# Kernel optimization log

Measured on AMD Instinct MI355X. Metric: run time of the kernel, lower is better.

## Reference

```python
import jax, jax.numpy as jnp
import numpy as np

EPS = 1e-8  # torch.cosine_similarity norm clamp

def setup_inputs() -> dict:
    key = jax.random.key(0)
    k1, k2, k3, k4 = jax.random.split(key, 4)
    B, S, D, C = 64, 512, 768, 512
    V = jax.random.normal(k1, (B, S, D), dtype=jnp.float32)
    label_embeddings = jax.random.normal(k2, (C, D), dtype=jnp.float32)
    fc_w = jax.random.normal(k3, (C, D), dtype=jnp.float32) * 0.02
    fc_b = jax.random.normal(k4, (C,), dtype=jnp.float32) * 0.02
    return {"V": V, "label_embeddings": label_embeddings, "fc_w": fc_w, "fc_b": fc_b}

def reference(V, label_embeddings, fc_w, fc_b):
    # Normalized embeddings (cosine similarity = dot of unit vectors, norms clamped at EPS)
    Vn = V / jnp.maximum(jnp.linalg.norm(V, axis=-1, keepdims=True), EPS)
    Ln = label_embeddings / jnp.maximum(
        jnp.linalg.norm(label_embeddings, axis=-1, keepdims=True), EPS)
    # [B, S, C] cosine similarities, then max over classes -> per-token weight m [B, S]
    sims = jnp.einsum('bsd,cd->bsc', Vn, Ln)
    m = jnp.max(sims, axis=-1)
    # Softmax over sequence dim -> attention beta [B, S]
    beta = jax.nn.softmax(m, axis=-1)
    # Weighted sum of token embeddings: z = V^T beta  -> [B, D]
    z = jnp.einsum('bsd,bs->bd', V, beta)
    # Final classifier
    out = z @ fc_w.T + fc_b
    return (out, z)
```

## Files before the change

### kernel.cpp

```cpp
#include <hip/hip_runtime.h>
#include <cstdint>
#include <cstddef>

#define BB 64
#define SS 512
#define DD 768
#define CC 512

typedef __attribute__((ext_vector_type(8))) short short8;
typedef __attribute__((ext_vector_type(4))) float f32x4;

#define GLOBAL_AS __attribute__((address_space(1)))
#define LDS_AS __attribute__((address_space(3)))

static __device__ __forceinline__ unsigned short f2bf(float f) {
  union { float f; unsigned u; } v; v.f = f;
  unsigned u = v.u;
  u += 0x7FFFu + ((u >> 16) & 1u);
  return (unsigned short)(u >> 16);
}
static __device__ __forceinline__ float bf2f(unsigned short u) {
  union { unsigned u; float f; } v; v.u = ((unsigned)u) << 16; return v.f;
}

static __device__ __forceinline__ void async_copy16(const void* g, void* l) {
  __builtin_amdgcn_global_load_lds((const GLOBAL_AS void*)g, (LDS_AS void*)l,
                                   16, 0, 0);
}

__global__ __launch_bounds__(256) void k_label_norm(const float* __restrict__ L,
                                                    unsigned short* __restrict__ Lnb) {
  const int c = blockIdx.x;
  const int tid = threadIdx.x;
  const float* row = L + (size_t)c * DD;
  float v[3];
  float s = 0.f;
#pragma unroll
  for (int k = 0; k < 3; k++) { v[k] = row[tid + 256 * k]; s += v[k] * v[k]; }
#pragma unroll
  for (int o = 32; o > 0; o >>= 1) s += __shfl_xor(s, o, 64);
  __shared__ float wsum[4];
  if ((tid & 63) == 0) wsum[tid >> 6] = s;
  __syncthreads();
  const float tot = wsum[0] + wsum[1] + wsum[2] + wsum[3];
  const float inv = 1.f / fmaxf(sqrtf(tot), 1e-8f);
  unsigned short* orow = Lnb + (size_t)c * DD;
  const int sw = c & 7;
#pragma unroll
  for (int k = 0; k < 3; k++) {
    const int d = tid + 256 * k;
    const int idx = (((d >> 3) ^ sw) << 3) | (d & 7);
    orow[idx] = f2bf(v[k] * inv);
  }
}

__global__ __launch_bounds__(256) void k_vprep(const float* __restrict__ V,
                                               unsigned short* __restrict__ Vb,
                                               float* __restrict__ inv_norm) {
  const int wave = threadIdx.x >> 6;
  const int lane = threadIdx.x & 63;
  const int tok = blockIdx.x * 4 + wave;
  const float* src = V + (size_t)tok * DD;
  unsigned short* dst = Vb + (size_t)tok * DD;
  float n2 = 0.f;
#pragma unroll
  for (int j = 0; j < 3; j++) {
    const int e = j * 256 + lane * 4;
    const float4 x = *(const float4*)(src + e);
    n2 += x.x * x.x + x.y * x.y + x.z * x.z + x.w * x.w;
    ushort4 o;
    o.x = f2bf(x.x); o.y = f2bf(x.y); o.z = f2bf(x.z); o.w = f2bf(x.w);
    *(ushort4*)(dst + e) = o;
  }
#pragma unroll
  for (int o = 32; o > 0; o >>= 1) n2 += __shfl_xor(n2, o, 64);
  if (lane == 0) inv_norm[tok] = 1.f / fmaxf(sqrtf(n2), 1e-8f);
}

__global__ __launch_bounds__(128, 2) void k_sims32(const unsigned short* __restrict__ Vb,
                                                   const float* __restrict__ inv_norm,
                                                   const unsigned short* __restrict__ Lnb,
                                                   float* __restrict__ em_out) {
  const int tid = threadIdx.x;
  const int wave = tid >> 6;
  const int lane = tid & 63;
  const int q = lane >> 4;
  const int mr = lane & 15;
  const int64_t tokBase = (int64_t)blockIdx.x * 64 + wave * 32;

  __shared__ unsigned short Bs[2][16 * DD];

  {
    const char* src = (const char*)Lnb;
    char* dst = (char*)&Bs[0][0];
#pragma unroll
    for (int j = 0; j < 12; j++) {
      const int i = wave + 2 * j;
      async_copy16(src + i * 1024 + lane * 16, dst + i * 1024);
    }
  }

  short8 afrag[2][24];
#pragma unroll
  for (int s = 0; s < 2; s++) {
    const short8* ap = (const short8*)(Vb + (tokBase + s * 16 + mr) * DD + q * 8);
#pragma unroll
    for (int kc = 0; kc < 24; kc++) afrag[s][kc] = ap[kc * 4];
  }

  __syncthreads();

  const int swLo = mr & 3;
  const int swHi = (mr >> 2) & 1;
  const int elemBase = mr * DD + ((q ^ swLo) << 3);
  const int u0off = swHi ? 32 : 0;
  const int u1off = swHi ? 0 : 32;

  f32x4 vmax0 = {-3e38f, -3e38f, -3e38f, -3e38f};
  f32x4 vmax1 = {-3e38f, -3e38f, -3e38f, -3e38f};
  for (int cc = 0; cc < 32; cc++) {
    const int p = cc & 1;
    if (cc + 1 < 32) {
      const char* src = (const char*)(Lnb + (size_t)(cc + 1) * 16 * DD);
      char* dst = (char*)&Bs[p ^ 1][0];
#pragma unroll
      for (int j = 0; j < 12; j++) {
        const int i = wave + 2 * j;
        async_copy16(src + i * 1024 + lane * 16, dst + i * 1024);
      }
    }
    const unsigned short* b0 = &Bs[p][elemBase + u0off];
    const unsigned short* b1 = &Bs[p][elemBase + u1off];
    f32x4 a0 = {0.f, 0.f, 0.f, 0.f};
    f32x4 a1 = {0.f, 0.f, 0.f, 0.f};
#pragma unroll
    for (int t = 0; t < 12; t++) {
      const short8 bu0 = *(const short8*)(b0 + t * 64);
      a0 = __builtin_amdgcn_mfma_f32_16x16x32_bf16(afrag[0][2 * t], bu0, a0, 0, 0, 0);
      a1 = __builtin_amdgcn_mfma_f32_16x16x32_bf16(afrag[1][2 * t], bu0, a1, 0, 0, 0);
      const short8 bu1 = *(const short8*)(b1 + t * 64);
      a0 = __builtin_amdgcn_mfma_f32_16x16x32_bf16(afrag[0][2 * t + 1], bu1, a0, 0, 0, 0);
      a1 = __builtin_amdgcn_mfma_f32_16x16x32_bf16(afrag[1][2 * t + 1], bu1, a1, 0, 0, 0);
    }
    vmax0[0] = fmaxf(vmax0[0], a0[0]); vmax0[1] = fmaxf(vmax0[1], a0[1]);
    vmax0[2] = fmaxf(vmax0[2], a0[2]); vmax0[3] = fmaxf(vmax0[3], a0[3]);
    vmax1[0] = fmaxf(vmax1[0], a1[0]); vmax1[1] = fmaxf(vmax1[1], a1[1]);
    vmax1[2] = fmaxf(vmax1[2], a1[2]); vmax1[3] = fmaxf(vmax1[3], a1[3]);
    __syncthreads();
  }
#pragma unroll
  for (int o = 1; o < 16; o <<= 1) {
#pragma unroll
    for (int r = 0; r < 4; r++) {
      vmax0[r] = fmaxf(vmax0[r], __shfl_xor(vmax0[r], o, 64));
      vmax1[r] = fmaxf(vmax1[r], __shfl_xor(vmax1[r], o, 64));
    }
  }
  if (mr == 0) {
#pragma unroll
    for (int r = 0; r < 4; r++) {
      const float i0 = inv_norm[tokBase + q * 4 + r];
      em_out[tokBase + q * 4 + r] = __expf(vmax0[r] * i0 - 1.f);
      const float i1 = inv_norm[tokBase + 16 + q * 4 + r];
      em_out[tokBase + 16 + q * 4 + r] = __expf(vmax1[r] * i1 - 1.f);
    }
  }
}

__global__ __launch_bounds__(256) void k_sims16(const float* __restrict__ V,
                                                const unsigned short* __restrict__ Lnb,
                                                float* __restrict__ em_out) {
  const int tid = threadIdx.x;
  const int wave = tid >> 6;
  const int lane = tid & 63;
  const int q = lane >> 4;
  const int mr = lane & 15;
  const int64_t tokBase = (int64_t)blockIdx.x * 64 + wave * 16;

  __shared__ unsigned short Bs[2][16 * DD];
  __shared__ float nrmS[4][16];

  {
    const char* src = (const char*)Lnb;
    char* dst = (char*)&Bs[0][0];
#pragma unroll
    for (int j = 0; j < 6; j++) {
      const int i = wave + 4 * j;
      async_copy16(src + i * 1024 + lane * 16, dst + i * 1024);
    }
  }
  const float* arow = V + (tokBase + mr) * DD + q * 8;
  short8 afrag[24];
  float nrm2 = 0.f;
#pragma unroll
  for (int kc = 0; kc < 24; kc++) {
    const float4* p = (const float4*)(arow + kc * 32);
    const float4 x = p[0];
    const float4 y = p[1];
    short8 a;
    a[0] = (short)f2bf(x.x); a[1] = (short)f2bf(x.y);
    a[2] = (short)f2bf(x.z); a[3] = (short)f2bf(x.w);
    a[4] = (short)f2bf(y.x); a[5] = (short)f2bf(y.y);
    a[6] = (short)f2bf(y.z); a[7] = (short)f2bf(y.w);
    afrag[kc] = a;
    nrm2 += x.x * x.x + x.y * x.y + x.z * x.z + x.w * x.w;
    nrm2 += y.x * y.x + y.y * y.y + y.z * y.z + y.w * y.w;
  }
  nrm2 += __shfl_xor(nrm2, 16, 64);
  nrm2 += __shfl_xor(nrm2, 32, 64);
  if (q == 0) nrmS[wave][mr] = nrm2;
  __syncthreads();

  const int swLo = mr & 3;
  const int swHi = (mr >> 2) & 1;
  const int elemBase = mr * DD + ((q ^ swLo) << 3);
  const int u0off = swHi ? 32 : 0;
  const int u1off = swHi ? 0 : 32;

  f32x4 vmax = {-3e38f, -3e38f, -3e38f, -3e38f};
  for (int cc = 0; cc < 32; cc++) {
    const int p = cc & 1;
    if (cc + 1 < 32) {
      const char* src = (const char*)(Lnb + (size_t)(cc + 1) * 16 * DD);
      char* dst = (char*)&Bs[p ^ 1][0];
#pragma unroll
      for (int j = 0; j < 6; j++) {
        const int i = wave + 4 * j;
        async_copy16(src + i * 1024 + lane * 16, dst + i * 1024);
      }
    }
    const unsigned short* b0 = &Bs[p][elemBase + u0off];
    const unsigned short* b1 = &Bs[p][elemBase + u1off];
    f32x4 acc = {0.f, 0.f, 0.f, 0.f};
#pragma unroll
    for (int t = 0; t < 12; t++) {
      const short8 bu0 = *(const short8*)(b0 + t * 64);
      acc = __builtin_amdgcn_mfma_f32_16x16x32_bf16(afrag[2 * t], bu0, acc, 0, 0, 0);
      const short8 bu1 = *(const short8*)(b1 + t * 64);
      acc = __builtin_amdgcn_mfma_f32_16x16x32_bf16(afrag[2 * t + 1], bu1, acc, 0, 0, 0);
    }
    vmax[0] = fmaxf(vmax[0], acc[0]);
    vmax[1] = fmaxf(vmax[1], acc[1]);
    vmax[2] = fmaxf(vmax[2], acc[2]);
    vmax[3] = fmaxf(vmax[3], acc[3]);
    __syncthreads();
  }
#pragma unroll
  for (int o = 1; o < 16; o <<= 1) {
#pragma unroll
    for (int r = 0; r < 4; r++) vmax[r] = fmaxf(vmax[r], __shfl_xor(vmax[r], o, 64));
  }
  if (mr == 0) {
#pragma unroll
    for (int r = 0; r < 4; r++) {
      const float nr = nrmS[wave][q * 4 + r];
      const float m = vmax[r] / fmaxf(sqrtf(nr), 1e-8f);
      em_out[tokBase + q * 4 + r] = __expf(m - 1.f);
    }
  }
}

__global__ __launch_bounds__(192) void k_zpart_bf(const unsigned short* __restrict__ Vb,
                                                  const float* __restrict__ em,
                                                  float* __restrict__ zpart,
                                                  int spc, int nsc) {
  const int blk = blockIdx.x;
  const int b = blk / nsc;
  const int sc = blk % nsc;
  const int tid = threadIdx.x;
  const unsigned short* vb = Vb + ((size_t)b * SS + (size_t)sc * spc) * DD + tid * 4;
  const float* bb = em + (size_t)b * SS + (size_t)sc * spc;
  float4 acc = {0.f, 0.f, 0.f, 0.f};
#pragma unroll 4
  for (int s = 0; s < spc; s++) {
    const float w = bb[s];
    const ushort4 u = *(const ushort4*)(vb + (size_t)s * DD);
    acc.x += w * bf2f(u.x); acc.y += w * bf2f(u.y);
    acc.z += w * bf2f(u.z); acc.w += w * bf2f(u.w);
  }
  *(float4*)(zpart + (size_t)blk * DD + tid * 4) = acc;
}

__global__ __launch_bounds__(192) void k_zpart_f32(const float* __restrict__ V,
                                                   const float* __restrict__ em,
                                                   float* __restrict__ zpart,
                                                   int spc, int nsc) {
  const int blk = blockIdx.x;
  const int b = blk / nsc;
  const int sc = blk % nsc;
  const int tid = threadIdx.x;
  const float* vb = V + ((size_t)b * SS + (size_t)sc * spc) * DD + tid * 4;
  const float* bb = em + (size_t)b * SS + (size_t)sc * spc;
  float4 acc = {0.f, 0.f, 0.f, 0.f};
#pragma unroll 4
  for (int s = 0; s < spc; s++) {
    const float w = bb[s];
    const float4 x = *(const float4*)(vb + (size_t)s * DD);
    acc.x += w * x.x; acc.y += w * x.y; acc.z += w * x.z; acc.w += w * x.w;
  }
  *(float4*)(zpart + (size_t)blk * DD + tid * 4) = acc;
}

__global__ __launch_bounds__(256) void k_final(const float* __restrict__ zpart,
                                               const float* __restrict__ em,
                                               const float* __restrict__ fc_w,
                                               const float* __restrict__ fc_b,
                                               float* __restrict__ out,
                                               float* __restrict__ zout,
                                               int nsc) {
  const int b = blockIdx.x >> 1;
  const int half = blockIdx.x & 1;
  const int tid = threadIdx.x;
  const float* eb = em + (size_t)b * SS;
  float es = eb[tid] + eb[tid + 256];
#pragma unroll
  for (int o = 32; o > 0; o >>= 1) es += __shfl_xor(es, o, 64);
  __shared__ float wred[4];
  if ((tid & 63) == 0) wred[tid >> 6] = es;
  __shared__ float zs[DD];
  __syncthreads();
  const float inv = 1.f / (wred[0] + wred[1] + wred[2] + wred[3]);
  for (int i = tid; i < DD; i += 256) {
    float s = 0.f;
    for (int sc = 0; sc < nsc; sc++) s += zpart[((size_t)b * nsc + sc) * DD + i];
    s *= inv;
    zs[i] = s;
    if (half == 0) zout[(size_t)b * DD + i] = s;
  }
  __syncthreads();
  const int c = half * 256 + tid;
  const float4* w = (const float4*)(fc_w + (size_t)c * DD);
  float acc = 0.f;
  for (int d4 = 0; d4 < DD / 4; d4++) {
    const float4 ww = w[d4];
    acc += ww.x * zs[d4 * 4] + ww.y * zs[d4 * 4 + 1] +
           ww.z * zs[d4 * 4 + 2] + ww.w * zs[d4 * 4 + 3];
  }
  out[(size_t)b * CC + c] = acc + fc_b[c];
}

extern "C" void kernel_launch(void* const* d_in, const int* in_sizes, int n_in,
                              void* d_out, int out_size, void* d_ws, size_t ws_size,
                              hipStream_t stream) {
  const float* V  = (const float*)d_in[0];
  const float* L  = (const float*)d_in[1];
  const float* fw = (const float*)d_in[2];
  const float* fb = (const float*)d_in[3];
  float* out = (float*)d_out;

  char* ws = (char*)d_ws;
  unsigned short* Lnb = (unsigned short*)ws;
  float* em       = (float*)(ws + 786432);
  float* inv_norm = (float*)(ws + 917504);
  unsigned short* Vb = (unsigned short*)(ws + 1048576);
  const size_t vb_bytes = (size_t)BB * SS * DD * 2;

  const size_t need16 = 1048576 + vb_bytes + (size_t)16 * BB * DD * 4;
  const bool big = ws_size >= need16;

  k_label_norm<<<CC, 256, 0, stream>>>(L, Lnb);
  if (big) {
    const int nsc = 16, spc = SS / nsc;
    float* zpart = (float*)(ws + 1048576 + vb_bytes);
    k_vprep<<<BB * SS / 4, 256, 0, stream>>>(V, Vb, inv_norm);
    k_sims32<<<512, 128, 0, stream>>>(Vb, inv_norm, Lnb, em);
    k_zpart_bf<<<BB * nsc, 192, 0, stream>>>(Vb, em, zpart, spc, nsc);
    k_final<<<2 * BB, 256, 0, stream>>>(zpart, em, fw, fb, out, out + BB * CC, nsc);
  } else {
    const int nsc = 8, spc = SS / nsc;
    float* zpart = (float*)(ws + 1048576);
    k_sims16<<<512, 256, 0, stream>>>(V, Lnb, em);
    k_zpart_f32<<<BB * nsc, 192, 0, stream>>>(V, em, zpart, spc, nsc);
    k_final<<<2 * BB, 256, 0, stream>>>(zpart, em, fw, fb, out, out + BB * CC, nsc);
  }
}
```

Measured before the change: 247.7 us.

## Split class dimension across wave halves in sims kernel; nontemporal V prep

The sims kernel becomes a 512-thread block covering 128 tokens, with two wave groups each scanning half of the label classes using their own double-buffered LDS tiles. Partial maxima are combined through shared memory before the exp is written. This halves the serial class loop per wave and launches 256 blocks instead of 512, trading more LDS per block and an extra barrier for shorter per-wave latency chains. The V prep kernel also switches to nontemporal loads and stores to avoid polluting the cache with streamed data.

```diff
diff --git a/kernel.cpp b/kernel.cpp
--- a/kernel.cpp
+++ b/kernel.cpp
@@ -9,6 +9,7 @@
 
 typedef __attribute__((ext_vector_type(8))) short short8;
 typedef __attribute__((ext_vector_type(4))) float f32x4;
+typedef __attribute__((ext_vector_type(4))) unsigned short u16x4;
 
 #define GLOBAL_AS __attribute__((address_space(1)))
 #define LDS_AS __attribute__((address_space(3)))
@@ -66,36 +67,39 @@
 #pragma unroll
   for (int j = 0; j < 3; j++) {
     const int e = j * 256 + lane * 4;
-    const float4 x = *(const float4*)(src + e);
-    n2 += x.x * x.x + x.y * x.y + x.z * x.z + x.w * x.w;
-    ushort4 o;
-    o.x = f2bf(x.x); o.y = f2bf(x.y); o.z = f2bf(x.z); o.w = f2bf(x.w);
-    *(ushort4*)(dst + e) = o;
+    const f32x4 x = __builtin_nontemporal_load((const f32x4*)(src + e));
+    n2 += x[0] * x[0] + x[1] * x[1] + x[2] * x[2] + x[3] * x[3];
+    u16x4 o;
+    o[0] = f2bf(x[0]); o[1] = f2bf(x[1]); o[2] = f2bf(x[2]); o[3] = f2bf(x[3]);
+    __builtin_nontemporal_store(o, (u16x4*)(dst + e));
   }
 #pragma unroll
   for (int o = 32; o > 0; o >>= 1) n2 += __shfl_xor(n2, o, 64);
   if (lane == 0) inv_norm[tok] = 1.f / fmaxf(sqrtf(n2), 1e-8f);
 }
 
-__global__ __launch_bounds__(128, 2) void k_sims32(const unsigned short* __restrict__ Vb,
-                                                   const float* __restrict__ inv_norm,
-                                                   const unsigned short* __restrict__ Lnb,
-                                                   float* __restrict__ em_out) {
+__global__ __launch_bounds__(512, 2) void k_sims_hs(const unsigned short* __restrict__ Vb,
+                                                    const float* __restrict__ inv_norm,
+                                                    const unsigned short* __restrict__ Lnb,
+                                                    float* __restrict__ em_out) {
   const int tid = threadIdx.x;
   const int wave = tid >> 6;
   const int lane = tid & 63;
   const int q = lane >> 4;
   const int mr = lane & 15;
-  const int64_t tokBase = (int64_t)blockIdx.x * 64 + wave * 32;
-
-  __shared__ unsigned short Bs[2][16 * DD];
+  const int h = wave >> 2;
+  const int wq = wave & 3;
+  const int64_t tokBase = (int64_t)blockIdx.x * 128 + wq * 32;
+
+  __shared__ unsigned short Bs[2][2][16 * DD];
+  __shared__ float mS[2][128];
 
   {
-    const char* src = (const char*)Lnb;
-    char* dst = (char*)&Bs[0][0];
-#pragma unroll
-    for (int j = 0; j < 12; j++) {
-      const int i = wave + 2 * j;
+    const char* src = (const char*)(Lnb + (size_t)(h * 16) * 16 * DD);
+    char* dst = (char*)&Bs[0][h][0];
+#pragma unroll
+    for (int j = 0; j < 6; j++) {
+      const int i = wq * 6 + j;
       async_copy16(src + i * 1024 + lane * 16, dst + i * 1024);
     }
   }
@@ -118,19 +122,19 @@
 
   f32x4 vmax0 = {-3e38f, -3e38f, -3e38f, -3e38f};
   f32x4 vmax1 = {-3e38f, -3e38f, -3e38f, -3e38f};
-  for (int cc = 0; cc < 32; cc++) {
+  for (int cc = 0; cc < 16; cc++) {
     const int p = cc & 1;
-    if (cc + 1 < 32) {
-      const char* src = (const char*)(Lnb + (size_t)(cc + 1) * 16 * DD);
-      char* dst = (char*)&Bs[p ^ 1][0];
-#pragma unroll
-      for (int j = 0; j < 12; j++) {
-        const int i = wave + 2 * j;
+    if (cc + 1 < 16) {
+      const char* src = (const char*)(Lnb + (size_t)(h * 16 + cc + 1) * 16 * DD);
+      char* dst = (char*)&Bs[p ^ 1][h][0];
+#pragma unroll
+      for (int j = 0; j < 6; j++) {
+        const int i = wq * 6 + j;
         async_copy16(src + i * 1024 + lane * 16, dst + i * 1024);
       }
     }
-    const unsigned short* b0 = &Bs[p][elemBase + u0off];
-    const unsigned short* b1 = &Bs[p][elemBase + u1off];
+    const unsigned short* b0 = &Bs[p][h][elemBase + u0off];
+    const unsigned short* b1 = &Bs[p][h][elemBase + u1off];
     f32x4 a0 = {0.f, 0.f, 0.f, 0.f};
     f32x4 a1 = {0.f, 0.f, 0.f, 0.f};
 #pragma unroll
@@ -159,10 +163,21 @@
   if (mr == 0) {
 #pragma unroll
     for (int r = 0; r < 4; r++) {
-      const float i0 = inv_norm[tokBase + q * 4 + r];
-      em_out[tokBase + q * 4 + r] = __expf(vmax0[r] * i0 - 1.f);
-      const float i1 = inv_norm[tokBase + 16 + q * 4 + r];
-      em_out[tokBase + 16 + q * 4 + r] = __expf(vmax1[r] * i1 - 1.f);
+      mS[h][wq * 32 + q * 4 + r] = vmax0[r];
+      mS[h][wq * 32 + 16 + q * 4 + r] = vmax1[r];
+    }
+  }
+  __syncthreads();
+  if (h == 0 && mr == 0) {
+#pragma unroll
+    for (int s = 0; s < 2; s++) {
+#pragma unroll
+      for (int r = 0; r < 4; r++) {
+        const int tl = wq * 32 + s * 16 + q * 4 + r;
+        const int64_t gt = (int64_t)blockIdx.x * 128 + tl;
+        const float m = fmaxf(mS[0][tl], mS[1][tl]) * inv_norm[gt];
+        em_out[gt] = __expf(m - 1.f);
+      }
     }
   }
 }
@@ -363,7 +378,7 @@
     const int nsc = 16, spc = SS / nsc;
     float* zpart = (float*)(ws + 1048576 + vb_bytes);
     k_vprep<<<BB * SS / 4, 256, 0, stream>>>(V, Vb, inv_norm);
-    k_sims32<<<512, 128, 0, stream>>>(Vb, inv_norm, Lnb, em);
+    k_sims_hs<<<256, 512, 0, stream>>>(Vb, inv_norm, Lnb, em);
     k_zpart_bf<<<BB * nsc, 192, 0, stream>>>(Vb, em, zpart, spc, nsc);
     k_final<<<2 * BB, 256, 0, stream>>>(zpart, em, fw, fb, out, out + BB * CC, nsc);
   } else {
```

Result: no change. 244.0 us (-1.5%).
